# Performance work log

Measured on AMD Instinct MI355X. Metric: run time of the kernel, lower is better.

## Reference

```python
import jax, jax.numpy as jnp
import numpy as np

EMBED = 1024
HEADS = 16
HEAD_DIM = EMBED // HEADS


def setup_inputs() -> dict:
    key = jax.random.key(0)
    ks = jax.random.split(key, 5)
    x = jax.random.normal(ks[0], (4, 2048, EMBED), dtype=jnp.float32)
    s = 1.0 / np.sqrt(EMBED)
    W_qkv = jax.random.normal(ks[1], (EMBED, 3 * EMBED), dtype=jnp.float32) * s
    b_qkv = jnp.zeros((3 * EMBED,), dtype=jnp.float32)
    W_proj = jax.random.normal(ks[2], (EMBED, EMBED), dtype=jnp.float32) * s
    b_proj = jnp.zeros((EMBED,), dtype=jnp.float32)
    return {"x": x, "W_qkv": W_qkv, "b_qkv": b_qkv, "W_proj": W_proj, "b_proj": b_proj}


def reference(x, W_qkv, b_qkv, W_proj, b_proj):
    B, S, E = x.shape
    scale = 1.0 / np.sqrt(HEAD_DIM)
    qkv = x @ W_qkv + b_qkv                      # [B,S,3E]
    qkv = qkv.reshape(B, S, 3, HEADS, HEAD_DIM)
    q, k, v = qkv[:, :, 0], qkv[:, :, 1], qkv[:, :, 2]   # [B,S,H,D]
    scores = jnp.einsum('bshd,bthd->bhst', q, k) * scale  # [B,H,S,S]
    attn = jax.nn.softmax(scores, axis=-1)
    out = jnp.einsum('bhst,bthd->bshd', attn, v)          # [B,S,H,D]
    out = out.reshape(B, S, E)
    return out @ W_proj + b_proj
```

## Files before the change

kernel.cpp:

```cpp
#include <hip/hip_runtime.h>
#include <math.h>

#define EMBED 1024
#define HEADS 16
#define HD    64
#define SEQ   2048
#define BATCH 4
#define ROWS  (BATCH * SEQ)

typedef _Float16 f16;
typedef __attribute__((ext_vector_type(8))) _Float16 f16x8;
typedef __attribute__((ext_vector_type(4))) _Float16 f16x4;
typedef __attribute__((ext_vector_type(2))) _Float16 f16x2;
typedef __attribute__((ext_vector_type(4))) float    fx4;

typedef __attribute__((address_space(3))) char  lds_char;
typedef __attribute__((address_space(1))) const char glb_char;

#define SCALE_Q 0.18033688011112042f

#define BAR_LGKM()  asm volatile("s_waitcnt lgkmcnt(0)\n\ts_barrier" ::: "memory")
#define BAR_VM8()   asm volatile("s_waitcnt vmcnt(8)\n\ts_barrier" ::: "memory")
#define BAR_VM6()   asm volatile("s_waitcnt vmcnt(6)\n\ts_barrier" ::: "memory")
#define BAR_VM0()   asm volatile("s_waitcnt vmcnt(0)\n\ts_barrier" ::: "memory")

__global__ __launch_bounds__(256) void prep(const float* __restrict__ x,
                                            f16* __restrict__ x_h,
                                            const float* __restrict__ Wqkv,
                                            f16* __restrict__ Wqt,
                                            const float* __restrict__ Wproj,
                                            f16* __restrict__ Wpt) {
    const int blk = blockIdx.x;
    if (blk < 8192) {
        const int i = (blk * 256 + threadIdx.x) * 4;
        const float4 v = *(const float4*)(x + i);
        f16x4 o = {(f16)v.x, (f16)v.y, (f16)v.z, (f16)v.w};
        *(f16x4*)(x_h + i) = o;
        return;
    }
    __shared__ float t[32][33];
    const float* W;
    f16* Wt;
    int N, bx, by;
    if (blk < 8192 + 3072) {
        const int b2 = blk - 8192;
        W = Wqkv; Wt = Wqt; N = 3072; bx = b2 % 96; by = b2 / 96;
    } else {
        const int b2 = blk - 8192 - 3072;
        W = Wproj; Wt = Wpt; N = 1024; bx = b2 % 32; by = b2 / 32;
    }
    const int tx = threadIdx.x & 31, ty = threadIdx.x >> 5;
    const int k0 = by * 32, n0 = bx * 32;
    #pragma unroll
    for (int i = 0; i < 4; i++)
        t[ty + i * 8][tx] = W[(size_t)(k0 + ty + i * 8) * N + n0 + tx];
    __syncthreads();
    #pragma unroll
    for (int i = 0; i < 4; i++)
        Wt[(size_t)(n0 + ty + i * 8) * 1024 + k0 + tx] = (f16)t[tx][ty + i * 8];
}

template <int MODE>
__global__ __launch_bounds__(256) void gemm_f16k(const f16* __restrict__ A,
                                                 const f16* __restrict__ Bt,
                                                 const float* __restrict__ bias,
                                                 float* __restrict__ Cf,
                                                 f16* __restrict__ qH,
                                                 f16* __restrict__ kH,
                                                 f16* __restrict__ vT,
                                                 int M, int N, int K) {
    constexpr int MI  = (MODE == 0) ? 2 : 4;
    constexpr int BM  = MI * 32;
    constexpr int AEL = BM * 64;
    constexpr int BEL = 128 * 64;
    __shared__ alignas(16) f16 smem[2 * (AEL + BEL)];

    f16 (*As0)[64] = (f16(*)[64])(smem);
    f16 (*As1)[64] = (f16(*)[64])(smem + AEL);
    f16 (*Bs0)[64] = (f16(*)[64])(smem + 2 * AEL);
    f16 (*Bs1)[64] = (f16(*)[64])(smem + 2 * AEL + BEL);
    lds_char* a0b = (lds_char*)smem;
    lds_char* a1b = (lds_char*)smem + 2 * AEL;
    lds_char* b0b = (lds_char*)smem + 4 * AEL;
    lds_char* b1b = (lds_char*)smem + 4 * AEL + 2 * BEL;

    const int tid  = threadIdx.x;
    const int wave = tid >> 6;
    const int lane = tid & 63;
    const int quad = lane >> 4;
    const int l16  = lane & 15;

    const int nwg  = gridDim.x * gridDim.y;
    const int flat = blockIdx.y * gridDim.x + blockIdx.x;
    const int swz  = (flat & 7) * (nwg >> 3) + (flat >> 3);
    const int bx   = swz % gridDim.x;
    const int by   = swz / gridDim.x;
    const int m0   = by * BM;
    const int n0   = bx * 128;
    const int wm   = wave & 1;
    const int wn   = wave >> 1;

    fx4 acc[MI][4];
    #pragma unroll
    for (int i = 0; i < MI; i++)
        #pragma unroll
        for (int j = 0; j < 4; j++)
            acc[i][j] = (fx4){0.f, 0.f, 0.f, 0.f};

    const int srow = lane >> 3;
    const int sjl  = ((lane & 7) ^ (srow & 7)) * 8;
    auto STAGE = [&](lds_char* asb, lds_char* bsb, int k0) {
        #pragma unroll
        for (int it = 0; it < MI; it++) {
            const int g = it * 4 + wave;
            const int r = g * 8 + srow;
            __builtin_amdgcn_global_load_lds(
                (glb_char*)(A + (size_t)(m0 + r) * K + k0 + sjl),
                asb + g * 1024, 16, 0, 0);
        }
        #pragma unroll
        for (int it = 0; it < 4; it++) {
            const int g = it * 4 + wave;
            const int r = g * 8 + srow;
            __builtin_amdgcn_global_load_lds(
                (glb_char*)(Bt + (size_t)(n0 + r) * K + k0 + sjl),
                bsb + g * 1024, 16, 0, 0);
        }
    };

    const int NT = K >> 6;

    auto ITER = [&](f16 (*As)[64], f16 (*Bs)[64],
                    lds_char* asb, lds_char* bsb, int t) {
        f16x8 af0[MI], af1[MI], bf0[4], bf1[4];
        #pragma unroll
        for (int i = 0; i < MI; i++) {
            const int ra = wm * (MI * 16) + i * 16 + l16;
            af0[i] = *(const f16x8*)&As[ra][((0 + quad) ^ (ra & 7)) * 8];
            af1[i] = *(const f16x8*)&As[ra][((4 + quad) ^ (ra & 7)) * 8];
        }
        #pragma unroll
        for (int j = 0; j < 4; j++) {
            const int rb = wn * 64 + j * 16 + l16;
            bf0[j] = *(const f16x8*)&Bs[rb][((0 + quad) ^ (rb & 7)) * 8];
            bf1[j] = *(const f16x8*)&Bs[rb][((4 + quad) ^ (rb & 7)) * 8];
        }
        BAR_LGKM();
        const bool more = (t + 2 < NT);
        if (more) STAGE(asb, bsb, (t + 2) * 64);
        __builtin_amdgcn_s_setprio(1);
        #pragma unroll
        for (int i = 0; i < MI; i++)
            #pragma unroll
            for (int j = 0; j < 4; j++) {
                acc[i][j] = __builtin_amdgcn_mfma_f32_16x16x32_f16(af0[i], bf0[j], acc[i][j], 0, 0, 0);
                acc[i][j] = __builtin_amdgcn_mfma_f32_16x16x32_f16(af1[i], bf1[j], acc[i][j], 0, 0, 0);
            }
        __builtin_amdgcn_s_setprio(0);
        if (more) { if constexpr (MODE == 0) BAR_VM6(); else BAR_VM8(); }
        else      BAR_VM0();
    };

    STAGE(a0b, b0b, 0);
    STAGE(a1b, b1b, 64);
    if constexpr (MODE == 0) BAR_VM6(); else BAR_VM8();

    for (int t = 0; t < NT; t += 2) {
        ITER(As0, Bs0, a0b, b0b, t);
        ITER(As1, Bs1, a1b, b1b, t + 1);
    }

    const int region = (MODE == 1) ? (n0 >> 10) : 0;

    if (MODE == 1 && region == 2) {
        const int b  = m0 >> 11;
        const int s0 = m0 & 2047;
        #pragma unroll
        for (int i = 0; i < MI; i++) {
            #pragma unroll
            for (int j = 0; j < 4; j++) {
                const int nloc = wn * 64 + j * 16 + l16;
                const float bn = bias[n0 + nloc];
                #pragma unroll
                for (int r = 0; r < 4; r++) {
                    const int sloc = wm * 64 + i * 16 + quad * 4 + r;
                    const int sp   = (sloc & ~31) | ((sloc & 15) << 1) | ((sloc >> 4) & 1);
                    const int phys = (sp >> 3) ^ (nloc & 15);
                    smem[nloc * 128 + phys * 8 + (sp & 7)] = (f16)(acc[i][j][r] + bn);
                }
            }
        }
        __syncthreads();
        const int nl = tid >> 1;
        const int hf = tid & 1;
        const int np0 = n0 - 2048;
        f16* dst = vT + ((size_t)(b * 16 + ((np0 + nl) >> 6)) * HD + (nl & 63)) * SEQ
                      + s0 + hf * 64;
        #pragma unroll
        for (int ch = 0; ch < 8; ch++) {
            const int lc   = hf * 8 + ch;
            const int phys = lc ^ (nl & 15);
            const f16x8 v  = *(const f16x8*)&smem[nl * 128 + phys * 8];
            *(f16x8*)(dst + ch * 8) = v;
        }
        return;
    }

    #pragma unroll
    for (int i = 0; i < MI; i++) {
        const int mb = m0 + wm * (MI * 16) + i * 16 + quad * 4;
        #pragma unroll
        for (int j = 0; j < 4; j++) {
            const int n  = n0 + wn * 64 + j * 16 + l16;
            const float bn = bias[n];
            #pragma unroll
            for (int r = 0; r < 4; r++) {
                const int m = mb + r;
                const float v = acc[i][j][r] + bn;
                if (MODE == 0) {
                    Cf[(size_t)m * N + n] = v;
                } else {
                    const int b = m >> 11, s = m & 2047;
                    if (region == 0) {
                        qH[(size_t)m * EMBED + n] = (f16)(v * SCALE_Q);
                    } else {
                        const int np = n - 1024, hh = np >> 6, d = np & 63;
                        kH[(((size_t)(b * 16 + hh) * SEQ + s) << 6) + d] = (f16)v;
                    }
                }
            }
        }
    }
}

__global__ __launch_bounds__(256, 4) void attn_mfma(const f16* __restrict__ qH,
                                                    const f16* __restrict__ kH,
                                                    const f16* __restrict__ vT,
                                                    f16* __restrict__ ctx) {
    __shared__ alignas(16) f16 Ks[64 * 64];
    __shared__ alignas(16) f16 Vt[64 * 64];
    __shared__ alignas(16) f16 Pl[4][2][16 * 64];

    const int tid  = threadIdx.x;
    const int wave = tid >> 6;
    const int lane = tid & 63;
    const int quad = lane >> 4;
    const int l16  = lane & 15;

    const int bid = (int)blockIdx.x;
    const int swz = (bid & 7) * 128 + (bid >> 3);
    const int qb = swz & 15;
    const int bh = swz >> 4;
    const int h  = bh & 15;
    const int b  = bh >> 4;
    const int q0 = qb * 128 + wave * 32;

    const f16* kB = kH + (size_t)bh * SEQ * HD;
    const f16* vB = vT + (size_t)bh * HD * SEQ;

    f16x8 qf[2][2];
    #pragma unroll
    for (int s = 0; s < 2; s++) {
        const f16* qp = qH + (size_t)(b * SEQ + q0 + s * 16 + l16) * EMBED + h * HD;
        #pragma unroll
        for (int c = 0; c < 2; c++)
            qf[s][c] = *(const f16x8*)(qp + c * 32 + quad * 8);
    }

    fx4 o[2][4];
    fx4 ls[2];
    #pragma unroll
    for (int s = 0; s < 2; s++) {
        ls[s] = (fx4){0.f, 0.f, 0.f, 0.f};
        #pragma unroll
        for (int dc = 0; dc < 4; dc++)
            o[s][dc] = (fx4){0.f, 0.f, 0.f, 0.f};
    }

    f16x8 ones8;
    #pragma unroll
    for (int j = 0; j < 8; j++) ones8[j] = (f16)1.0f;

    lds_char* ksb = (lds_char*)&Ks[0];
    lds_char* vsb = (lds_char*)&Vt[0];

    auto STAGE_K = [&](int kb) {
        #pragma unroll
        for (int it = 0; it < 2; it++) {
            const int g  = wave * 2 + it;
            const int c  = g * 64 + lane;
            const int r  = c >> 3;
            const int jl = (c & 7) ^ (r & 7);
            __builtin_amdgcn_global_load_lds(
                (glb_char*)(kB + (size_t)(kb * 64 + r) * HD + jl * 8),
                ksb + g * 1024, 16, 0, 0);
        }
    };
    auto STAGE_V = [&](int kb) {
        #pragma unroll
        for (int it = 0; it < 2; it++) {
            const int g  = wave * 2 + it;
            const int c  = g * 64 + lane;
            const int r  = c >> 3;
            const int jl = (c & 7) ^ (r & 7);
            __builtin_amdgcn_global_load_lds(
                (glb_char*)(vB + (size_t)r * SEQ + kb * 64 + jl * 8),
                vsb + g * 1024, 16, 0, 0);
        }
    };

    STAGE_K(0);
    STAGE_V(0);
    __syncthreads();

    for (int kb = 0; kb < SEQ / 64; kb++) {
        fx4 st0[4], st1[4];
        __builtin_amdgcn_s_setprio(1);
        #pragma unroll
        for (int t = 0; t < 4; t++) {
            const int row = l16 + 16 * t;
            const f16x8 kt0 = *(const f16x8*)&Ks[(row * 8 + ((0 + quad) ^ (row & 7))) * 8];
            const f16x8 kt1 = *(const f16x8*)&Ks[(row * 8 + ((4 + quad) ^ (row & 7))) * 8];
            fx4 z = {0.f, 0.f, 0.f, 0.f};
            st0[t] = __builtin_amdgcn_mfma_f32_16x16x32_f16(qf[0][0], kt0, z, 0, 0, 0);
            st0[t] = __builtin_amdgcn_mfma_f32_16x16x32_f16(qf[0][1], kt1, st0[t], 0, 0, 0);
            st1[t] = __builtin_amdgcn_mfma_f32_16x16x32_f16(qf[1][0], kt0, z, 0, 0, 0);
            st1[t] = __builtin_amdgcn_mfma_f32_16x16x32_f16(qf[1][1], kt1, st1[t], 0, 0, 0);
        }
        __builtin_amdgcn_s_setprio(0);

        #pragma unroll
        for (int g = 0; g < 2; g++)
            #pragma unroll
            for (int r = 0; r < 4; r++) {
                const int row = quad * 4 + r;
                const int cc  = (g * 4 + (l16 >> 2)) ^ (row & 7);
                {
                    const float pa = __builtin_amdgcn_exp2f(st0[2 * g][r]);
                    const float pb = __builtin_amdgcn_exp2f(st0[2 * g + 1][r]);
                    const f16x2 pk = __builtin_bit_cast(f16x2, __builtin_amdgcn_cvt_pkrtz(pa, pb));
                    *(f16x2*)&Pl[wave][0][row * 64 + cc * 8 + (l16 & 3) * 2] = pk;
                }
                {
                    const float pa = __builtin_amdgcn_exp2f(st1[2 * g][r]);
                    const float pb = __builtin_amdgcn_exp2f(st1[2 * g + 1][r]);
                    const f16x2 pk = __builtin_bit_cast(f16x2, __builtin_amdgcn_cvt_pkrtz(pa, pb));
                    *(f16x2*)&Pl[wave][1][row * 64 + cc * 8 + (l16 & 3) * 2] = pk;
                }
            }

        __syncthreads();
        if (kb + 1 < SEQ / 64) STAGE_K(kb + 1);

        const f16x8 pf00 = *(const f16x8*)&Pl[wave][0][l16 * 64 + ((0 + quad) ^ (l16 & 7)) * 8];
        const f16x8 pf01 = *(const f16x8*)&Pl[wave][0][l16 * 64 + ((4 + quad) ^ (l16 & 7)) * 8];
        const f16x8 pf10 = *(const f16x8*)&Pl[wave][1][l16 * 64 + ((0 + quad) ^ (l16 & 7)) * 8];
        const f16x8 pf11 = *(const f16x8*)&Pl[wave][1][l16 * 64 + ((4 + quad) ^ (l16 & 7)) * 8];
        __builtin_amdgcn_s_setprio(1);
        #pragma unroll
        for (int dc = 0; dc < 4; dc++) {
            const int row = 16 * dc + l16;
            const f16x8 vf0 = *(const f16x8*)&Vt[(row * 8 + ((0 + quad) ^ (row & 7))) * 8];
            const f16x8 vf1 = *(const f16x8*)&Vt[(row * 8 + ((4 + quad) ^ (row & 7))) * 8];
            o[0][dc] = __builtin_amdgcn_mfma_f32_16x16x32_f16(pf00, vf0, o[0][dc], 0, 0, 0);
            o[0][dc] = __builtin_amdgcn_mfma_f32_16x16x32_f16(pf01, vf1, o[0][dc], 0, 0, 0);
            o[1][dc] = __builtin_amdgcn_mfma_f32_16x16x32_f16(pf10, vf0, o[1][dc], 0, 0, 0);
            o[1][dc] = __builtin_amdgcn_mfma_f32_16x16x32_f16(pf11, vf1, o[1][dc], 0, 0, 0);
        }
        ls[0] = __builtin_amdgcn_mfma_f32_16x16x32_f16(pf00, ones8, ls[0], 0, 0, 0);
        ls[0] = __builtin_amdgcn_mfma_f32_16x16x32_f16(pf01, ones8, ls[0], 0, 0, 0);
        ls[1] = __builtin_amdgcn_mfma_f32_16x16x32_f16(pf10, ones8, ls[1], 0, 0, 0);
        ls[1] = __builtin_amdgcn_mfma_f32_16x16x32_f16(pf11, ones8, ls[1], 0, 0, 0);
        __builtin_amdgcn_s_setprio(0);

        __syncthreads();
        if (kb + 1 < SEQ / 64) STAGE_V(kb + 1);
    }

    #pragma unroll
    for (int s = 0; s < 2; s++) {
        #pragma unroll
        for (int r = 0; r < 4; r++) {
            const float inv = 1.0f / ls[s][r];
            const int q = q0 + s * 16 + quad * 4 + r;
            f16* dst = ctx + (size_t)(b * SEQ + q) * EMBED + h * HD;
            #pragma unroll
            for (int dc = 0; dc < 4; dc++)
                dst[dc * 16 + l16] = (f16)(o[s][dc][r] * inv);
        }
    }
}

extern "C" void kernel_launch(void* const* d_in, const int* in_sizes, int n_in,
                              void* d_out, int out_size, void* d_ws, size_t ws_size,
                              hipStream_t stream) {
    const float* x     = (const float*)d_in[0];
    const float* Wqkv  = (const float*)d_in[1];
    const float* bqkv  = (const float*)d_in[2];
    const float* Wproj = (const float*)d_in[3];
    const float* bproj = (const float*)d_in[4];
    float* out = (float*)d_out;

    f16* x_h = (f16*)d_ws;
    f16* qHb = x_h + (size_t)ROWS * EMBED;
    f16* kHb = qHb + (size_t)ROWS * EMBED;
    f16* vTb = kHb + (size_t)ROWS * EMBED;
    f16* ctx = vTb + (size_t)ROWS * EMBED;
    f16* Wqt = ctx + (size_t)ROWS * EMBED;
    f16* Wpt = Wqt + (size_t)3 * EMBED * EMBED;

    prep<<<dim3(12288), dim3(256), 0, stream>>>(x, x_h, Wqkv, Wqt, Wproj, Wpt);

    gemm_f16k<1><<<dim3(3 * EMBED / 128, ROWS / 128), dim3(256), 0, stream>>>(
        x_h, Wqt, bqkv, nullptr, qHb, kHb, vTb, ROWS, 3 * EMBED, EMBED);

    attn_mfma<<<dim3(64 * 16), dim3(256), 0, stream>>>(qHb, kHb, vTb, ctx);

    gemm_f16k<0><<<dim3(EMBED / 128, ROWS / 64), dim3(256), 0, stream>>>(
        ctx, Wpt, bproj, out, nullptr, nullptr, nullptr, ROWS, EMBED, EMBED);
}
```

Baseline: 264.1 us.

## Split GEMM tiles across eight waves per block instead of four

Both GEMM kernels now launch 512-thread blocks with the same output tile. Each wave computes a smaller sub-tile (2 by BJ MFMA blocks), and the global-to-LDS staging loads and vmcnt thresholds are rescaled to match. The V-transpose epilogue pads the LDS row stride to 136 and uses four threads per row. The aim is more resident waves to hide memory and barrier latency, at the cost of fewer MFMAs per LDS fragment load and costlier block-wide barriers.

```diff
diff --git a/kernel.cpp b/kernel.cpp
--- a/kernel.cpp
+++ b/kernel.cpp
@@ -20,8 +20,8 @@
 #define SCALE_Q 0.18033688011112042f
 
 #define BAR_LGKM()  asm volatile("s_waitcnt lgkmcnt(0)\n\ts_barrier" ::: "memory")
-#define BAR_VM8()   asm volatile("s_waitcnt vmcnt(8)\n\ts_barrier" ::: "memory")
-#define BAR_VM6()   asm volatile("s_waitcnt vmcnt(6)\n\ts_barrier" ::: "memory")
+#define BAR_VM4()   asm volatile("s_waitcnt vmcnt(4)\n\ts_barrier" ::: "memory")
+#define BAR_VM3()   asm volatile("s_waitcnt vmcnt(3)\n\ts_barrier" ::: "memory")
 #define BAR_VM0()   asm volatile("s_waitcnt vmcnt(0)\n\ts_barrier" ::: "memory")
 
 __global__ __launch_bounds__(256) void prep(const float* __restrict__ x,
@@ -61,7 +61,7 @@
 }
 
 template <int MODE>
-__global__ __launch_bounds__(256) void gemm_f16k(const f16* __restrict__ A,
+__global__ __launch_bounds__(512) void gemm_f16k(const f16* __restrict__ A,
                                                  const f16* __restrict__ Bt,
                                                  const float* __restrict__ bias,
                                                  float* __restrict__ Cf,
@@ -69,8 +69,11 @@
                                                  f16* __restrict__ kH,
                                                  f16* __restrict__ vT,
                                                  int M, int N, int K) {
-    constexpr int MI  = (MODE == 0) ? 2 : 4;
-    constexpr int BM  = MI * 32;
+    constexpr int BM  = (MODE == 0) ? 64 : 128;
+    constexpr int WMS = (MODE == 0) ? 2 : 4;
+    constexpr int WNS = 8 / WMS;
+    constexpr int AI  = 2;
+    constexpr int BJ  = 128 / (WNS * 16);
     constexpr int AEL = BM * 64;
     constexpr int BEL = 128 * 64;
     __shared__ alignas(16) f16 smem[2 * (AEL + BEL)];
@@ -97,30 +100,30 @@
     const int by   = swz / gridDim.x;
     const int m0   = by * BM;
     const int n0   = bx * 128;
-    const int wm   = wave & 1;
-    const int wn   = wave >> 1;
-
-    fx4 acc[MI][4];
-    #pragma unroll
-    for (int i = 0; i < MI; i++)
-        #pragma unroll
-        for (int j = 0; j < 4; j++)
+    const int wm   = wave % WMS;
+    const int wn   = wave / WMS;
+
+    fx4 acc[AI][BJ];
+    #pragma unroll
+    for (int i = 0; i < AI; i++)
+        #pragma unroll
+        for (int j = 0; j < BJ; j++)
             acc[i][j] = (fx4){0.f, 0.f, 0.f, 0.f};
 
     const int srow = lane >> 3;
     const int sjl  = ((lane & 7) ^ (srow & 7)) * 8;
     auto STAGE = [&](lds_char* asb, lds_char* bsb, int k0) {
         #pragma unroll
-        for (int it = 0; it < MI; it++) {
-            const int g = it * 4 + wave;
+        for (int it = 0; it < BM / 64; it++) {
+            const int g = it * 8 + wave;
             const int r = g * 8 + srow;
             __builtin_amdgcn_global_load_lds(
                 (glb_char*)(A + (size_t)(m0 + r) * K + k0 + sjl),
                 asb + g * 1024, 16, 0, 0);
         }
         #pragma unroll
-        for (int it = 0; it < 4; it++) {
-            const int g = it * 4 + wave;
+        for (int it = 0; it < 2; it++) {
+            const int g = it * 8 + wave;
             const int r = g * 8 + srow;
             __builtin_amdgcn_global_load_lds(
                 (glb_char*)(Bt + (size_t)(n0 + r) * K + k0 + sjl),
@@ -132,16 +135,16 @@
 
     auto ITER = [&](f16 (*As)[64], f16 (*Bs)[64],
                     lds_char* asb, lds_char* bsb, int t) {
-        f16x8 af0[MI], af1[MI], bf0[4], bf1[4];
-        #pragma unroll
-        for (int i = 0; i < MI; i++) {
-            const int ra = wm * (MI * 16) + i * 16 + l16;
+        f16x8 af0[AI], af1[AI], bf0[BJ], bf1[BJ];
+        #pragma unroll
+        for (int i = 0; i < AI; i++) {
+            const int ra = wm * (AI * 16) + i * 16 + l16;
             af0[i] = *(const f16x8*)&As[ra][((0 + quad) ^ (ra & 7)) * 8];
             af1[i] = *(const f16x8*)&As[ra][((4 + quad) ^ (ra & 7)) * 8];
         }
         #pragma unroll
-        for (int j = 0; j < 4; j++) {
-            const int rb = wn * 64 + j * 16 + l16;
+        for (int j = 0; j < BJ; j++) {
+            const int rb = wn * (BJ * 16) + j * 16 + l16;
             bf0[j] = *(const f16x8*)&Bs[rb][((0 + quad) ^ (rb & 7)) * 8];
             bf1[j] = *(const f16x8*)&Bs[rb][((4 + quad) ^ (rb & 7)) * 8];
         }
@@ -150,20 +153,20 @@
         if (more) STAGE(asb, bsb, (t + 2) * 64);
         __builtin_amdgcn_s_setprio(1);
         #pragma unroll
-        for (int i = 0; i < MI; i++)
+        for (int i = 0; i < AI; i++)
             #pragma unroll
-            for (int j = 0; j < 4; j++) {
+            for (int j = 0; j < BJ; j++) {
                 acc[i][j] = __builtin_amdgcn_mfma_f32_16x16x32_f16(af0[i], bf0[j], acc[i][j], 0, 0, 0);
                 acc[i][j] = __builtin_amdgcn_mfma_f32_16x16x32_f16(af1[i], bf1[j], acc[i][j], 0, 0, 0);
             }
         __builtin_amdgcn_s_setprio(0);
-        if (more) { if constexpr (MODE == 0) BAR_VM6(); else BAR_VM8(); }
+        if (more) { if constexpr (MODE == 0) BAR_VM3(); else BAR_VM4(); }
         else      BAR_VM0();
     };
 
     STAGE(a0b, b0b, 0);
     STAGE(a1b, b1b, 64);
-    if constexpr (MODE == 0) BAR_VM6(); else BAR_VM8();
+    if constexpr (MODE == 0) BAR_VM3(); else BAR_VM4();
 
     for (int t = 0; t < NT; t += 2) {
         ITER(As0, Bs0, a0b, b0b, t);
@@ -176,42 +179,41 @@
         const int b  = m0 >> 11;
         const int s0 = m0 & 2047;
         #pragma unroll
-        for (int i = 0; i < MI; i++) {
+        for (int i = 0; i < AI; i++) {
             #pragma unroll
-            for (int j = 0; j < 4; j++) {
-                const int nloc = wn * 64 + j * 16 + l16;
+            for (int j = 0; j < BJ; j++) {
+                const int nloc = wn * (BJ * 16) + j * 16 + l16;
                 const float bn = bias[n0 + nloc];
                 #pragma unroll
                 for (int r = 0; r < 4; r++) {
-                    const int sloc = wm * 64 + i * 16 + quad * 4 + r;
+                    const int sloc = wm * (AI * 16) + i * 16 + quad * 4 + r;
                     const int sp   = (sloc & ~31) | ((sloc & 15) << 1) | ((sloc >> 4) & 1);
                     const int phys = (sp >> 3) ^ (nloc & 15);
-                    smem[nloc * 128 + phys * 8 + (sp & 7)] = (f16)(acc[i][j][r] + bn);
+                    smem[nloc * 136 + phys * 8 + (sp & 7)] = (f16)(acc[i][j][r] + bn);
                 }
             }
         }
         __syncthreads();
-        const int nl = tid >> 1;
-        const int hf = tid & 1;
+        const int nl = tid >> 2;
+        const int qc = tid & 3;
         const int np0 = n0 - 2048;
-        f16* dst = vT + ((size_t)(b * 16 + ((np0 + nl) >> 6)) * HD + (nl & 63)) * SEQ
-                      + s0 + hf * 64;
-        #pragma unroll
-        for (int ch = 0; ch < 8; ch++) {
-            const int lc   = hf * 8 + ch;
+        f16* dst = vT + ((size_t)(b * 16 + ((np0 + nl) >> 6)) * HD + (nl & 63)) * SEQ + s0;
+        #pragma unroll
+        for (int ch = 0; ch < 4; ch++) {
+            const int lc   = qc * 4 + ch;
             const int phys = lc ^ (nl & 15);
-            const f16x8 v  = *(const f16x8*)&smem[nl * 128 + phys * 8];
-            *(f16x8*)(dst + ch * 8) = v;
+            const f16x8 v  = *(const f16x8*)&smem[nl * 136 + phys * 8];
+            *(f16x8*)(dst + lc * 8) = v;
         }
         return;
     }
 
     #pragma unroll
-    for (int i = 0; i < MI; i++) {
-        const int mb = m0 + wm * (MI * 16) + i * 16 + quad * 4;
-        #pragma unroll
-        for (int j = 0; j < 4; j++) {
-            const int n  = n0 + wn * 64 + j * 16 + l16;
+    for (int i = 0; i < AI; i++) {
+        const int mb = m0 + wm * (AI * 16) + i * 16 + quad * 4;
+        #pragma unroll
+        for (int j = 0; j < BJ; j++) {
+            const int n  = n0 + wn * (BJ * 16) + j * 16 + l16;
             const float bn = bias[n];
             #pragma unroll
             for (int r = 0; r < 4; r++) {
@@ -411,11 +413,11 @@
 
     prep<<<dim3(12288), dim3(256), 0, stream>>>(x, x_h, Wqkv, Wqt, Wproj, Wpt);
 
-    gemm_f16k<1><<<dim3(3 * EMBED / 128, ROWS / 128), dim3(256), 0, stream>>>(
+    gemm_f16k<1><<<dim3(3 * EMBED / 128, ROWS / 128), dim3(512), 0, stream>>>(
         x_h, Wqt, bqkv, nullptr, qHb, kHb, vTb, ROWS, 3 * EMBED, EMBED);
 
     attn_mfma<<<dim3(64 * 16), dim3(256), 0, stream>>>(qHb, kHb, vTb, ctx);
 
-    gemm_f16k<0><<<dim3(EMBED / 128, ROWS / 64), dim3(256), 0, stream>>>(
+    gemm_f16k<0><<<dim3(EMBED / 128, ROWS / 64), dim3(512), 0, stream>>>(
         ctx, Wpt, bproj, out, nullptr, nullptr, nullptr, ROWS, EMBED, EMBED);
 }
```

Measured after the change: 270.4 us. 1.02x slower.
